# Kernel tuning notes

Measured on AMD Instinct MI355X. Metric: run time of the kernel, lower is better.

The kernel has to match this reference:

```python
import jax, jax.numpy as jnp
import numpy as np

N = 500_000      # nodes
E = 4_000_000    # edges (avg degree 8)
F_IN = 24        # n_input (includeHeading=False, coords=False)
H = 64           # n_hidden
K = 6            # K_block Chebyshev order
OUT = 6          # n_output
EPS = 1e-5       # BatchNorm eps


def setup_inputs() -> dict:
    key = jax.random.key(0)
    ks = jax.random.split(key, 8)
    x = jax.random.normal(ks[0], (N, F_IN), dtype=jnp.float32)
    edge_index = jax.random.randint(ks[1], (2, E), 0, N, dtype=jnp.int32)
    # ChebConv(24 -> 64, K=6): stacked per-order weights [K, F_IN, H] + bias
    W1 = jax.random.normal(ks[2], (K, F_IN, H), dtype=jnp.float32) * (1.0 / np.sqrt(F_IN))
    b1 = jnp.zeros((H,), dtype=jnp.float32)
    # BatchNorm1d(64) affine params
    gamma = jnp.ones((H,), dtype=jnp.float32)
    beta = jnp.zeros((H,), dtype=jnp.float32)
    # conv_mix ChebConv(64 -> 6, K=1)
    Wmix = jax.random.normal(ks[3], (1, H, OUT), dtype=jnp.float32) * (1.0 / np.sqrt(H))
    bmix = jnp.zeros((OUT,), dtype=jnp.float32)
    return {"x": x, "edge_index": edge_index, "W1": W1, "b1": b1,
            "gamma": gamma, "beta": beta, "Wmix": Wmix, "bmix": bmix}


def cheb_conv(x, edge_index, W, b):
    """PyG ChebConv with normalization='sym', lambda_max=2.
    L_hat = L - I = -D^{-1/2} A D^{-1/2} (zero diagonal).
    """
    Kk = W.shape[0]
    row, col = edge_index[0], edge_index[1]  # messages flow row -> col
    deg = jax.ops.segment_sum(jnp.ones((E,), x.dtype), col, num_segments=N)
    dis = jnp.where(deg > 0, jax.lax.rsqrt(jnp.maximum(deg, 1.0)), 0.0)
    norm = -(dis[row] * dis[col])  # [E]

    def prop(h):  # h: [N, F] -> L_hat @ h via gather-scale-scatter
        return jax.ops.segment_sum(norm[:, None] * h[row], col, num_segments=N)

    Tx0 = x
    out = Tx0 @ W[0]
    if Kk > 1:
        Tx1 = prop(Tx0)
        out = out + Tx1 @ W[1]
        for k in range(2, Kk):
            Tx2 = 2.0 * prop(Tx1) - Tx0
            out = out + Tx2 @ W[k]
            Tx0, Tx1 = Tx1, Tx2
    return out + b


def reference(x, edge_index, W1, b1, gamma, beta, Wmix, bmix):
    # Kipfblock: ChebConv -> BatchNorm1d (batch stats) -> ReLU
    h = cheb_conv(x, edge_index, W1, b1)            # [N, H]
    mean = jnp.mean(h, axis=0)
    var = jnp.mean(jnp.square(h - mean), axis=0)    # biased var, as torch BN training
    h = (h - mean) * jax.lax.rsqrt(var + EPS) * gamma + beta
    h = jax.nn.relu(h)
    # conv_mix: ChebConv K=1 reduces to a dense linear (T_0 = x only)
    y = h @ Wmix[0] + bmix                          # [N, OUT]
    # F.dropout is identity in eval mode
    return y
```

## Files before the change

kernel.cpp:

```cpp
#include <hip/hip_runtime.h>
#include <hip/hip_fp16.h>

#define NN 500000
#define NE 4000000
#define FI 24
#define FH 64
#define KC 6
#define FO 6
#define BN_EPS 1e-5f

#define SLOTS 32
#define RH 32
#define NMT (NN / 16)
#define PASS_GRID 1024

#define EPT 8
#define CHUNK (256 * EPT)
#define NCHUNK ((NE + CHUNK - 1) / CHUNK)

#define BUCKETS 512
#define BW 977
#define BCAP 15500

#define RMASK 0x7FFFFu

typedef _Float16 half8 __attribute__((ext_vector_type(8)));
typedef float f32x4 __attribute__((ext_vector_type(4)));
typedef int int4v __attribute__((ext_vector_type(4)));
union U4H8 { uint4 u; half8 h; };


__device__ __forceinline__ void acc8(float* a, float d, uint4 u) {
    const __half2* h2 = (const __half2*)&u;
    #pragma unroll
    for (int j = 0; j < 4; ++j) {
        float2 f = __half22float2(h2[j]);
        a[2 * j]     += d * f.x;
        a[2 * j + 1] += d * f.y;
    }
}

__device__ __forceinline__ uint4 pack8(const float* a) {
    uint4 u;
    __half2* h2 = (__half2*)&u;
    #pragma unroll
    for (int j = 0; j < 4; ++j) h2[j] = __floats2half2_rn(a[2 * j], a[2 * j + 1]);
    return u;
}


__global__ __launch_bounds__(256) void k_scatter(
    const int* __restrict__ row, const int* __restrict__ col,
    unsigned int* __restrict__ ebuf, int* __restrict__ cur) {
    __shared__ unsigned int val[CHUNK];
    __shared__ unsigned short bk[CHUNK];
    __shared__ int hist[BUCKETS], base[BUCKETS], rk[BUCKETS];
    for (int t = threadIdx.x; t < BUCKETS; t += 256) { hist[t] = 0; rk[t] = 0; }
    __syncthreads();
    const int b0 = blockIdx.x * CHUNK;
    #pragma unroll
    for (int i = 0; i < EPT / 4; ++i) {
        int li4 = (i * 256 + threadIdx.x) * 4;
        int e0 = b0 + li4;
        if (e0 + 4 <= NE) {
            int4v c4 = *(const int4v*)(col + e0);
            int4v r4 = *(const int4v*)(row + e0);
            #pragma unroll
            for (int j = 0; j < 4; ++j) {
                int c = c4[j], r = r4[j];
                int b = c / BW, cl = c - b * BW;
                val[li4 + j] = (unsigned int)r | ((unsigned int)cl << 19);
                bk[li4 + j] = (unsigned short)b;
                atomicAdd(&hist[b], 1);
            }
        } else {
            for (int j = 0; j < 4; ++j) {
                int e = e0 + j, li = li4 + j;
                if (e < NE) {
                    int c = col[e], r = row[e];
                    int b = c / BW, cl = c - b * BW;
                    val[li] = (unsigned int)r | ((unsigned int)cl << 19);
                    bk[li] = (unsigned short)b;
                    atomicAdd(&hist[b], 1);
                } else {
                    bk[li] = 0xFFFF;
                }
            }
        }
    }
    __syncthreads();
    for (int t = threadIdx.x; t < BUCKETS; t += 256) {
        int n = hist[t];
        base[t] = n ? atomicAdd(&cur[t], n) : 0;
    }
    __syncthreads();
    #pragma unroll
    for (int i = 0; i < EPT / 4; ++i) {
        int li4 = (i * 256 + threadIdx.x) * 4;
        #pragma unroll
        for (int j = 0; j < 4; ++j) {
            int li = li4 + j;
            int b = bk[li];
            if (b != 0xFFFF) {
                int rkk = atomicAdd(&rk[b], 1);
                int pos = base[b] + rkk;
                if (pos < BCAP) ebuf[(size_t)b * BCAP + pos] = val[li];
            }
        }
    }
}


__global__ __launch_bounds__(256) void k_build(
    const unsigned int* __restrict__ ebuf, const int* __restrict__ cur,
    int* __restrict__ cnt, int* __restrict__ csrcT) {
    __shared__ int cl_cnt[BW];
    const int b = blockIdx.x;
    const int nbase = b * BW;
    const int width = (NN - nbase < BW) ? (NN - nbase) : BW;
    for (int i = threadIdx.x; i < BW; i += 256) cl_cnt[i] = 0;
    __syncthreads();
    int nb = cur[b];
    if (nb > BCAP) nb = BCAP;
    for (int i = threadIdx.x; i < nb; i += 256) {
        unsigned int v = ebuf[(size_t)b * BCAP + i];
        int cl = v >> 19;
        int r = v & RMASK;
        int pos = atomicAdd(&cl_cnt[cl], 1);
        if (pos < SLOTS) csrcT[(size_t)pos * NN + nbase + cl] = r;
    }
    __syncthreads();
    for (int i = threadIdx.x; i < width; i += 256) cnt[nbase + i] = cl_cnt[i];
}

__global__ void k_dis(const int* __restrict__ cnt, float* __restrict__ dis) {
    int n = blockIdx.x * blockDim.x + threadIdx.x;
    if (n < NN) {
        int d = cnt[n];
        dis[n] = d > 0 ? rsqrtf((float)d) : 0.0f;
    }
}


__global__ __launch_bounds__(256) void k_pack(
    const int* __restrict__ cnt, unsigned int* __restrict__ csrcT) {
    int n = blockIdx.x * 256 + threadIdx.x;
    if (n >= NN) return;
    int deg = cnt[n];
    if (deg > SLOTS) deg = SLOTS;
    for (int s = 0; s < deg; ++s) {
        size_t idx = (size_t)s * NN + n;
        unsigned int r = csrcT[idx] & RMASK;
        int dg = cnt[r];
        if (dg > 8191) dg = 8191;
        csrcT[idx] = r | ((unsigned int)dg << 19);
    }
}


__global__ void k_xhalf(const float* __restrict__ x, __half* __restrict__ Th0) {
    int n = blockIdx.x * blockDim.x + threadIdx.x;
    if (n >= NN) return;
    const float* r = x + (size_t)n * FI;
    float v[24];
    #pragma unroll
    for (int i = 0; i < 6; ++i) {
        float4 f = ((const float4*)r)[i];
        v[4 * i] = f.x; v[4 * i + 1] = f.y; v[4 * i + 2] = f.z; v[4 * i + 3] = f.w;
    }
    uint4* o = (uint4*)(Th0 + (size_t)n * RH);
    o[0] = pack8(v); o[1] = pack8(v + 8); o[2] = pack8(v + 16);
    o[3] = make_uint4(0, 0, 0, 0);
}


template<bool FIRST>
__global__ __launch_bounds__(256) void k_prop(
    const int* __restrict__ cnt, const unsigned int* __restrict__ csrcT,
    const float* __restrict__ dis,
    const __half* __restrict__ Tin, const __half* __restrict__ Tpp,
    __half* __restrict__ Tout) {
    int n = blockIdx.x * 256 + threadIdx.x;
    if (n >= NN) return;
    int deg = cnt[n];
    if (deg > SLOTS) deg = SLOTS;
    float a[24];
    #pragma unroll
    for (int j = 0; j < 24; ++j) a[j] = 0.0f;
    int s = 0;
    for (; s + 2 <= deg; s += 2) {
        unsigned int e0 = csrcT[(size_t)s * NN + n];
        unsigned int e1 = csrcT[(size_t)(s + 1) * NN + n];
        unsigned int r0 = e0 & RMASK, r1 = e1 & RMASK;
        unsigned int g0 = e0 >> 19,  g1 = e1 >> 19;
        float d0 = g0 ? rsqrtf((float)g0) : 0.0f;
        float d1 = g1 ? rsqrtf((float)g1) : 0.0f;
        const uint4* p0 = (const uint4*)(Tin + (size_t)r0 * RH);
        const uint4* p1 = (const uint4*)(Tin + (size_t)r1 * RH);
        uint4 u00 = p0[0], u01 = p0[1], u02 = p0[2];
        uint4 u10 = p1[0], u11 = p1[1], u12 = p1[2];
        acc8(a, d0, u00); acc8(a + 8, d0, u01); acc8(a + 16, d0, u02);
        acc8(a, d1, u10); acc8(a + 8, d1, u11); acc8(a + 16, d1, u12);
    }
    if (s < deg) {
        unsigned int e0 = csrcT[(size_t)s * NN + n];
        unsigned int r0 = e0 & RMASK;
        unsigned int g0 = e0 >> 19;
        float d0 = g0 ? rsqrtf((float)g0) : 0.0f;
        const uint4* p0 = (const uint4*)(Tin + (size_t)r0 * RH);
        acc8(a, d0, p0[0]); acc8(a + 8, d0, p0[1]); acc8(a + 16, d0, p0[2]);
    }
    float m = FIRST ? -dis[n] : -2.0f * dis[n];
    if (FIRST) {
        #pragma unroll
        for (int j = 0; j < 24; ++j) a[j] *= m;
    } else {
        const uint4* pr = (const uint4*)(Tpp + (size_t)n * RH);
        uint4 p0 = pr[0], p1 = pr[1], p2 = pr[2];
        float pv[24];
        {
            const __half2* h2 = (const __half2*)&p0;
            #pragma unroll
            for (int j = 0; j < 4; ++j) { float2 f = __half22float2(h2[j]); pv[2*j] = f.x; pv[2*j+1] = f.y; }
        }
        {
            const __half2* h2 = (const __half2*)&p1;
            #pragma unroll
            for (int j = 0; j < 4; ++j) { float2 f = __half22float2(h2[j]); pv[8+2*j] = f.x; pv[8+2*j+1] = f.y; }
        }
        {
            const __half2* h2 = (const __half2*)&p2;
            #pragma unroll
            for (int j = 0; j < 4; ++j) { float2 f = __half22float2(h2[j]); pv[16+2*j] = f.x; pv[16+2*j+1] = f.y; }
        }
        #pragma unroll
        for (int j = 0; j < 24; ++j) a[j] = m * a[j] - pv[j];
    }
    uint4* o = (uint4*)(Tout + (size_t)n * RH);
    o[0] = pack8(a); o[1] = pack8(a + 8); o[2] = pack8(a + 16);
    o[3] = make_uint4(0, 0, 0, 0);
}


__device__ __forceinline__ void build_bfrags(const float* __restrict__ W1, uint4* Bf) {
    for (int s = threadIdx.x; s < KC * 4 * 64; s += 256) {
        int lane = s & 63, blk = s >> 6;
        int seg = blk >> 2, nb = blk & 3;
        int q = lane >> 4, n = lane & 15;
        float v[8];
        #pragma unroll
        for (int j = 0; j < 8; ++j) {
            int k = q * 8 + j;
            v[j] = (k < FI) ? W1[(seg * FI + k) * FH + nb * 16 + n] : 0.0f;
        }
        U4H8 u;
        __half2* h2 = (__half2*)&u;
        #pragma unroll
        for (int j = 0; j < 4; ++j) h2[j] = __floats2half2_rn(v[2 * j], v[2 * j + 1]);
        Bf[s] = u.u;
    }
}

__global__ __launch_bounds__(256) void k_pass1(
    const __half* __restrict__ Th, const float* __restrict__ W1,
    const float* __restrict__ b1, float* __restrict__ stats,
    __half* __restrict__ h) {
    __shared__ uint4 Bf[KC * 4 * 64];
    __shared__ float st[2 * FH];
    build_bfrags(W1, Bf);
    if (threadIdx.x < 2 * FH) st[threadIdx.x] = 0.0f;
    __syncthreads();
    const int lane = threadIdx.x & 63;
    const int q = lane >> 4, ln = lane & 15;
    const int wid = blockIdx.x * 4 + (threadIdx.x >> 6);
    const int nw = gridDim.x * 4;
    float bias[4];
    #pragma unroll
    for (int nb = 0; nb < 4; ++nb) bias[nb] = b1[nb * 16 + ln];
    float ssum[4] = {0, 0, 0, 0}, sqsum[4] = {0, 0, 0, 0};
    for (int t = wid; t < NMT; t += nw) {
        const int n0 = t * 16;
        f32x4 acc[4];
        #pragma unroll
        for (int nb = 0; nb < 4; ++nb)
            acc[nb] = (f32x4){bias[nb], bias[nb], bias[nb], bias[nb]};
        #pragma unroll
        for (int seg = 0; seg < KC; ++seg) {
            U4H8 a;
            a.u = *(const uint4*)(Th + (size_t)seg * ((size_t)NN * RH)
                                  + (size_t)(n0 + ln) * RH + q * 8);
            #pragma unroll
            for (int nb = 0; nb < 4; ++nb) {
                U4H8 b; b.u = Bf[(seg * 4 + nb) * 64 + lane];
                acc[nb] = __builtin_amdgcn_mfma_f32_16x16x32_f16(a.h, b.h, acc[nb], 0, 0, 0);
            }
        }
        #pragma unroll
        for (int nb = 0; nb < 4; ++nb) {
            #pragma unroll
            for (int r = 0; r < 4; ++r) {
                float v = acc[nb][r];
                ssum[nb] += v;
                sqsum[nb] += v * v;
                h[(size_t)(n0 + q * 4 + r) * FH + nb * 16 + ln] = __float2half(v);
            }
        }
    }
    #pragma unroll
    for (int nb = 0; nb < 4; ++nb) {
        ssum[nb]  += __shfl_xor(ssum[nb], 16);  ssum[nb]  += __shfl_xor(ssum[nb], 32);
        sqsum[nb] += __shfl_xor(sqsum[nb], 16); sqsum[nb] += __shfl_xor(sqsum[nb], 32);
    }
    if (lane < 16) {
        #pragma unroll
        for (int nb = 0; nb < 4; ++nb) {
            atomicAdd(&st[nb * 16 + ln], ssum[nb]);
            atomicAdd(&st[FH + nb * 16 + ln], sqsum[nb]);
        }
    }
    __syncthreads();
    if (threadIdx.x < 2 * FH) atomicAdd(&stats[threadIdx.x], st[threadIdx.x]);
}

__global__ void k_finalize(const float* __restrict__ stats, const float* __restrict__ gamma,
                           const float* __restrict__ beta, float* __restrict__ ss) {
    int f = threadIdx.x;
    if (f < FH) {
        float mean = stats[f] * (1.0f / NN);
        float var  = stats[f + FH] * (1.0f / NN) - mean * mean;
        float rstd = rsqrtf(var + BN_EPS);
        float sc = gamma[f] * rstd;
        ss[f] = sc;
        ss[f + FH] = beta[f] - mean * sc;
    }
}


__global__ __launch_bounds__(256) void k_pass2(
    const __half* __restrict__ h, const float* __restrict__ ss,
    const float* __restrict__ Wmix, const float* __restrict__ bmix,
    float* __restrict__ y) {
    __shared__ float tab[FH * 8];
    for (int f = threadIdx.x; f < FH; f += 256) {
        tab[f * 8 + 0] = ss[f];
        tab[f * 8 + 1] = ss[FH + f];
        #pragma unroll
        for (int o = 0; o < FO; ++o) tab[f * 8 + 2 + o] = Wmix[f * FO + o];
    }
    __syncthreads();
    int n = blockIdx.x * 256 + threadIdx.x;
    if (n >= NN) return;
    const uint4* hr = (const uint4*)(h + (size_t)n * FH);
    float p[FO];
    #pragma unroll
    for (int o = 0; o < FO; ++o) p[o] = bmix[o];
    #pragma unroll
    for (int blk = 0; blk < 8; ++blk) {
        U4H8 u; u.u = hr[blk];
        const __half2* h2 = (const __half2*)&u;
        #pragma unroll
        for (int j = 0; j < 4; ++j) {
            float2 f2 = __half22float2(h2[j]);
            int f = blk * 8 + j * 2;
            {
                float4 t0 = *(const float4*)&tab[f * 8];
                float4 t1 = *(const float4*)&tab[f * 8 + 4];
                float hv = fmaxf(f2.x * t0.x + t0.y, 0.0f);
                p[0] += hv * t0.z; p[1] += hv * t0.w;
                p[2] += hv * t1.x; p[3] += hv * t1.y;
                p[4] += hv * t1.z; p[5] += hv * t1.w;
            }
            {
                float4 t0 = *(const float4*)&tab[(f + 1) * 8];
                float4 t1 = *(const float4*)&tab[(f + 1) * 8 + 4];
                float hv = fmaxf(f2.y * t0.x + t0.y, 0.0f);
                p[0] += hv * t0.z; p[1] += hv * t0.w;
                p[2] += hv * t1.x; p[3] += hv * t1.y;
                p[4] += hv * t1.z; p[5] += hv * t1.w;
            }
        }
    }
    float* yo = y + (size_t)n * FO;
    #pragma unroll
    for (int o = 0; o < FO; ++o) yo[o] = p[o];
}


extern "C" void kernel_launch(void* const* d_in, const int* in_sizes, int n_in,
                              void* d_out, int out_size, void* d_ws, size_t ws_size,
                              hipStream_t stream) {
    const float* x     = (const float*)d_in[0];
    const int*   edge  = (const int*)d_in[1];
    const float* W1    = (const float*)d_in[2];
    const float* b1    = (const float*)d_in[3];
    const float* gamma = (const float*)d_in[4];
    const float* beta  = (const float*)d_in[5];
    const float* Wmix  = (const float*)d_in[6];
    const float* bmix  = (const float*)d_in[7];
    float* y = (float*)d_out;

    const int* row = edge;
    const int* col = edge + NE;

    const size_t O_CNT   = 0;
    const size_t O_DIS   = 500000;
    const size_t O_STATS = 1000000;
    const size_t O_SS    = 1000128;
    const size_t O_CSRC  = 1000256;
    const size_t O_TH    = 17000256;
    const size_t TOTAL_ELEMS = O_TH + 6ull * NN * RH / 2;
    if (ws_size < TOTAL_ELEMS * 4ull) return;

    float* wf = (float*)d_ws;
    int*   wi = (int*)d_ws;
    int*   cnt   = wi + O_CNT;
    float* dis   = wf + O_DIS;
    float* stats = wf + O_STATS;
    float* ss    = wf + O_SS;
    int*   csrcT = wi + O_CSRC;
    __half* hbuf = (__half*)(wi + O_CSRC);
    __half* Th   = (__half*)(wf + O_TH);
    __half* Th0  = Th;
    __half* Th1  = Th + 1ull * NN * RH;
    __half* Th2  = Th + 2ull * NN * RH;
    __half* Th3  = Th + 3ull * NN * RH;
    __half* Th4  = Th + 4ull * NN * RH;
    __half* Th5  = Th + 5ull * NN * RH;

    unsigned int* ebuf = (unsigned int*)Th5;
    int* cur = (int*)(ebuf + (size_t)BUCKETS * BCAP);

    (void)hipMemsetAsync(cur,   0, BUCKETS * sizeof(int), stream);
    (void)hipMemsetAsync(stats, 0, 128 * sizeof(float), stream);

    const int BS = 256;
    const int GN = (NN + BS - 1) / BS;

    k_scatter<<<NCHUNK, BS, 0, stream>>>(row, col, ebuf, cur);
    k_build<<<BUCKETS, BS, 0, stream>>>(ebuf, cur, cnt, csrcT);
    k_dis<<<GN, BS, 0, stream>>>(cnt, dis);
    k_pack<<<GN, BS, 0, stream>>>(cnt, (unsigned int*)csrcT);
    k_xhalf<<<GN, BS, 0, stream>>>(x, Th0);

    k_prop<true ><<<GN, BS, 0, stream>>>(cnt, (const unsigned int*)csrcT, dis, Th0, nullptr, Th1);
    k_prop<false><<<GN, BS, 0, stream>>>(cnt, (const unsigned int*)csrcT, dis, Th1, Th0, Th2);
    k_prop<false><<<GN, BS, 0, stream>>>(cnt, (const unsigned int*)csrcT, dis, Th2, Th1, Th3);
    k_prop<false><<<GN, BS, 0, stream>>>(cnt, (const unsigned int*)csrcT, dis, Th3, Th2, Th4);
    k_prop<false><<<GN, BS, 0, stream>>>(cnt, (const unsigned int*)csrcT, dis, Th4, Th3, Th5);

    k_pass1<<<PASS_GRID, 256, 0, stream>>>(Th, W1, b1, stats, hbuf);
    k_finalize<<<1, 64, 0, stream>>>(stats, gamma, beta, ss);
    k_pass2<<<GN, 256, 0, stream>>>(hbuf, ss, Wmix, bmix, y);
}
```

Baseline: 765.5 us.

## Renumber nodes by in-degree so prop threads in a wave share loop length

Result: slower. 1.407 ms (+83.9%).

```diff
diff --git a/kernel.cpp b/kernel.cpp
--- a/kernel.cpp
+++ b/kernel.cpp
@@ -12,7 +12,7 @@
 #define SLOTS 32
 #define RH 32
 #define NMT (NN / 16)
-#define PASS_GRID 1024
+#define PASS_GRID 2048
 
 #define EPT 8
 #define CHUNK (256 * EPT)
@@ -20,7 +20,7 @@
 
 #define BUCKETS 512
 #define BW 977
-#define BCAP 15500
+#define NBIN 33
 
 #define RMASK 0x7FFFFu
 
@@ -49,8 +49,90 @@
 }
 
 
+__global__ __launch_bounds__(256) void k_deg(
+    const int* __restrict__ col, int* __restrict__ cnt_raw) {
+    int e0 = (blockIdx.x * 256 + threadIdx.x) * 4;
+    if (e0 + 4 <= NE) {
+        int4v c4 = *(const int4v*)(col + e0);
+        #pragma unroll
+        for (int j = 0; j < 4; ++j) atomicAdd(&cnt_raw[c4[j]], 1);
+    } else {
+        for (int j = 0; j < 4; ++j)
+            if (e0 + j < NE) atomicAdd(&cnt_raw[col[e0 + j]], 1);
+    }
+}
+
+__global__ __launch_bounds__(256) void k_hist(
+    const int* __restrict__ cnt_raw, int* __restrict__ bins) {
+    __shared__ int lb[NBIN];
+    if (threadIdx.x < NBIN) lb[threadIdx.x] = 0;
+    __syncthreads();
+    int n = blockIdx.x * 256 + threadIdx.x;
+    if (n < NN) {
+        int d = cnt_raw[n];
+        if (d > 32) d = 32;
+        atomicAdd(&lb[d], 1);
+    }
+    __syncthreads();
+    if (threadIdx.x < NBIN && lb[threadIdx.x])
+        atomicAdd(&bins[threadIdx.x], lb[threadIdx.x]);
+}
+
+__global__ void k_scan(const int* __restrict__ bins, int* __restrict__ binbase) {
+    if (threadIdx.x == 0) {
+        int acc = 0;
+        for (int i = 0; i < NBIN; ++i) { binbase[i] = acc; acc += bins[i]; }
+    }
+}
+
+__global__ __launch_bounds__(256) void k_rank(
+    const int* __restrict__ cnt_raw, const int* __restrict__ binbase,
+    int* __restrict__ binoff, int* __restrict__ rank, int* __restrict__ bedges) {
+    __shared__ int lc[NBIN], lbase[NBIN];
+    if (threadIdx.x < NBIN) { lc[threadIdx.x] = 0; lbase[threadIdx.x] = 0; }
+    __syncthreads();
+    int n = blockIdx.x * 256 + threadIdx.x;
+    int d = 0, de = 0, lpos = 0;
+    bool valid = (n < NN);
+    if (valid) {
+        de = cnt_raw[n];
+        d = de > 32 ? 32 : de;
+        lpos = atomicAdd(&lc[d], 1);
+    }
+    __syncthreads();
+    if (threadIdx.x < NBIN && lc[threadIdx.x])
+        lbase[threadIdx.x] = atomicAdd(&binoff[threadIdx.x], lc[threadIdx.x]);
+    __syncthreads();
+    if (valid) {
+        int rid = binbase[d] + lbase[d] + lpos;
+        rank[n] = rid;
+        atomicAdd(&bedges[rid / BW], de);
+    }
+}
+
+__global__ __launch_bounds__(512) void k_scan2(
+    const int* __restrict__ bedges, int* __restrict__ bbase, int* __restrict__ cur) {
+    __shared__ int s[BUCKETS];
+    int t = threadIdx.x;
+    int own = bedges[t];
+    s[t] = own;
+    __syncthreads();
+    for (int off = 1; off < BUCKETS; off <<= 1) {
+        int v = (t >= off) ? s[t - off] : 0;
+        __syncthreads();
+        s[t] += v;
+        __syncthreads();
+    }
+    int excl = s[t] - own;
+    bbase[t] = excl;
+    cur[t] = excl;
+    if (t == BUCKETS - 1) bbase[BUCKETS] = s[t];
+}
+
+
 __global__ __launch_bounds__(256) void k_scatter(
     const int* __restrict__ row, const int* __restrict__ col,
+    const int* __restrict__ rank,
     unsigned int* __restrict__ ebuf, int* __restrict__ cur) {
     __shared__ unsigned int val[CHUNK];
     __shared__ unsigned short bk[CHUNK];
@@ -67,9 +149,10 @@
             int4v r4 = *(const int4v*)(row + e0);
             #pragma unroll
             for (int j = 0; j < 4; ++j) {
-                int c = c4[j], r = r4[j];
-                int b = c / BW, cl = c - b * BW;
-                val[li4 + j] = (unsigned int)r | ((unsigned int)cl << 19);
+                int rc = rank[c4[j]];
+                int rr = rank[r4[j]];
+                int b = rc / BW, cl = rc - b * BW;
+                val[li4 + j] = (unsigned int)rr | ((unsigned int)cl << 19);
                 bk[li4 + j] = (unsigned short)b;
                 atomicAdd(&hist[b], 1);
             }
@@ -77,9 +160,10 @@
             for (int j = 0; j < 4; ++j) {
                 int e = e0 + j, li = li4 + j;
                 if (e < NE) {
-                    int c = col[e], r = row[e];
-                    int b = c / BW, cl = c - b * BW;
-                    val[li] = (unsigned int)r | ((unsigned int)cl << 19);
+                    int rc = rank[col[e]];
+                    int rr = rank[row[e]];
+                    int b = rc / BW, cl = rc - b * BW;
+                    val[li] = (unsigned int)rr | ((unsigned int)cl << 19);
                     bk[li] = (unsigned short)b;
                     atomicAdd(&hist[b], 1);
                 } else {
@@ -102,9 +186,8 @@
             int li = li4 + j;
             int b = bk[li];
             if (b != 0xFFFF) {
-                int rkk = atomicAdd(&rk[b], 1);
-                int pos = base[b] + rkk;
-                if (pos < BCAP) ebuf[(size_t)b * BCAP + pos] = val[li];
+                int pos = base[b] + atomicAdd(&rk[b], 1);
+                if (pos < NE) ebuf[pos] = val[li];
             }
         }
     }
@@ -112,22 +195,21 @@
 
 
 __global__ __launch_bounds__(256) void k_build(
-    const unsigned int* __restrict__ ebuf, const int* __restrict__ cur,
+    const unsigned int* __restrict__ ebuf, const int* __restrict__ bbase,
     int* __restrict__ cnt, int* __restrict__ csrcT) {
     __shared__ int cl_cnt[BW];
-    const int b = blockIdx.x;
+    const int b = (BUCKETS - 1) - (int)blockIdx.x;
     const int nbase = b * BW;
     const int width = (NN - nbase < BW) ? (NN - nbase) : BW;
     for (int i = threadIdx.x; i < BW; i += 256) cl_cnt[i] = 0;
     __syncthreads();
-    int nb = cur[b];
-    if (nb > BCAP) nb = BCAP;
-    for (int i = threadIdx.x; i < nb; i += 256) {
-        unsigned int v = ebuf[(size_t)b * BCAP + i];
+    const int beg = bbase[b], end = bbase[b + 1];
+    for (int i = beg + threadIdx.x; i < end; i += 256) {
+        unsigned int v = ebuf[i];
         int cl = v >> 19;
-        int r = v & RMASK;
+        int rr = v & RMASK;
         int pos = atomicAdd(&cl_cnt[cl], 1);
-        if (pos < SLOTS) csrcT[(size_t)pos * NN + nbase + cl] = r;
+        if (pos < SLOTS) csrcT[(size_t)pos * NN + nbase + cl] = rr;
     }
     __syncthreads();
     for (int i = threadIdx.x; i < width; i += 256) cnt[nbase + i] = cl_cnt[i];
@@ -140,7 +222,6 @@
         dis[n] = d > 0 ? rsqrtf((float)d) : 0.0f;
     }
 }
-
 
 __global__ __launch_bounds__(256) void k_pack(
     const int* __restrict__ cnt, unsigned int* __restrict__ csrcT) {
@@ -157,8 +238,8 @@
     }
 }
 
-
-__global__ void k_xhalf(const float* __restrict__ x, __half* __restrict__ Th0) {
+__global__ void k_xhalf(const float* __restrict__ x, const int* __restrict__ rank,
+                        __half* __restrict__ Th0) {
     int n = blockIdx.x * blockDim.x + threadIdx.x;
     if (n >= NN) return;
     const float* r = x + (size_t)n * FI;
@@ -168,11 +249,11 @@
         float4 f = ((const float4*)r)[i];
         v[4 * i] = f.x; v[4 * i + 1] = f.y; v[4 * i + 2] = f.z; v[4 * i + 3] = f.w;
     }
-    uint4* o = (uint4*)(Th0 + (size_t)n * RH);
+    int rid = rank[n];
+    uint4* o = (uint4*)(Th0 + (size_t)rid * RH);
     o[0] = pack8(v); o[1] = pack8(v + 8); o[2] = pack8(v + 16);
     o[3] = make_uint4(0, 0, 0, 0);
 }
-
 
 template<bool FIRST>
 __global__ __launch_bounds__(256) void k_prop(
@@ -241,7 +322,6 @@
     o[3] = make_uint4(0, 0, 0, 0);
 }
 
-
 __device__ __forceinline__ void build_bfrags(const float* __restrict__ W1, uint4* Bf) {
     for (int s = threadIdx.x; s < KC * 4 * 64; s += 256) {
         int lane = s & 63, blk = s >> 6;
@@ -335,9 +415,9 @@
     }
 }
 
-
 __global__ __launch_bounds__(256) void k_pass2(
-    const __half* __restrict__ h, const float* __restrict__ ss,
+    const __half* __restrict__ h, const int* __restrict__ rank,
+    const float* __restrict__ ss,
     const float* __restrict__ Wmix, const float* __restrict__ bmix,
     float* __restrict__ y) {
     __shared__ float tab[FH * 8];
@@ -350,7 +430,8 @@
     __syncthreads();
     int n = blockIdx.x * 256 + threadIdx.x;
     if (n >= NN) return;
-    const uint4* hr = (const uint4*)(h + (size_t)n * FH);
+    int rid = rank[n];
+    const uint4* hr = (const uint4*)(h + (size_t)rid * FH);
     float p[FO];
     #pragma unroll
     for (int o = 0; o < FO; ++o) p[o] = bmix[o];
@@ -406,18 +487,35 @@
     const size_t O_DIS   = 500000;
     const size_t O_STATS = 1000000;
     const size_t O_SS    = 1000128;
-    const size_t O_CSRC  = 1000256;
-    const size_t O_TH    = 17000256;
-    const size_t TOTAL_ELEMS = O_TH + 6ull * NN * RH / 2;
+    const size_t O_AUX   = 1000256;
+    const size_t A_CNTRAW  = O_AUX;
+    const size_t A_RANK    = O_AUX + 500000;
+    const size_t A_BINS    = O_AUX + 1000000;
+    const size_t A_BINBASE = O_AUX + 1000064;
+    const size_t A_BINOFF  = O_AUX + 1000128;
+    const size_t A_BEDGES  = O_AUX + 1000192;
+    const size_t A_BBASE   = O_AUX + 1000704;
+    const size_t A_CUR     = O_AUX + 1001232;
+    const size_t O_CSRC  = O_AUX + 1001760;
+    const size_t O_TH    = O_CSRC + 16000000;
+    const size_t TOTAL_ELEMS = O_TH + 24000000;
     if (ws_size < TOTAL_ELEMS * 4ull) return;
 
     float* wf = (float*)d_ws;
     int*   wi = (int*)d_ws;
-    int*   cnt   = wi + O_CNT;
-    float* dis   = wf + O_DIS;
-    float* stats = wf + O_STATS;
-    float* ss    = wf + O_SS;
-    int*   csrcT = wi + O_CSRC;
+    int*   cnt     = wi + O_CNT;
+    float* dis     = wf + O_DIS;
+    float* stats   = wf + O_STATS;
+    float* ss      = wf + O_SS;
+    int*   cnt_raw = wi + A_CNTRAW;
+    int*   rank    = wi + A_RANK;
+    int*   bins    = wi + A_BINS;
+    int*   binbase = wi + A_BINBASE;
+    int*   binoff  = wi + A_BINOFF;
+    int*   bedges  = wi + A_BEDGES;
+    int*   bbase   = wi + A_BBASE;
+    int*   cur     = wi + A_CUR;
+    int*   csrcT   = wi + O_CSRC;
     __half* hbuf = (__half*)(wi + O_CSRC);
     __half* Th   = (__half*)(wf + O_TH);
     __half* Th0  = Th;
@@ -428,19 +526,27 @@
     __half* Th5  = Th + 5ull * NN * RH;
 
     unsigned int* ebuf = (unsigned int*)Th5;
-    int* cur = (int*)(ebuf + (size_t)BUCKETS * BCAP);
-
-    (void)hipMemsetAsync(cur,   0, BUCKETS * sizeof(int), stream);
-    (void)hipMemsetAsync(stats, 0, 128 * sizeof(float), stream);
+
+    (void)hipMemsetAsync(cnt_raw, 0, NN * sizeof(int), stream);
+    (void)hipMemsetAsync(bins,    0, 64 * sizeof(int), stream);
+    (void)hipMemsetAsync(binoff,  0, 64 * sizeof(int), stream);
+    (void)hipMemsetAsync(bedges,  0, 512 * sizeof(int), stream);
+    (void)hipMemsetAsync(stats,   0, 128 * sizeof(float), stream);
 
     const int BS = 256;
     const int GN = (NN + BS - 1) / BS;
-
-    k_scatter<<<NCHUNK, BS, 0, stream>>>(row, col, ebuf, cur);
-    k_build<<<BUCKETS, BS, 0, stream>>>(ebuf, cur, cnt, csrcT);
+    const int GD = (NE / 4 + BS - 1) / BS;
+
+    k_deg<<<GD, BS, 0, stream>>>(col, cnt_raw);
+    k_hist<<<GN, BS, 0, stream>>>(cnt_raw, bins);
+    k_scan<<<1, 64, 0, stream>>>(bins, binbase);
+    k_rank<<<GN, BS, 0, stream>>>(cnt_raw, binbase, binoff, rank, bedges);
+    k_scan2<<<1, 512, 0, stream>>>(bedges, bbase, cur);
+    k_scatter<<<NCHUNK, BS, 0, stream>>>(row, col, rank, ebuf, cur);
+    k_build<<<BUCKETS, BS, 0, stream>>>(ebuf, bbase, cnt, csrcT);
     k_dis<<<GN, BS, 0, stream>>>(cnt, dis);
     k_pack<<<GN, BS, 0, stream>>>(cnt, (unsigned int*)csrcT);
-    k_xhalf<<<GN, BS, 0, stream>>>(x, Th0);
+    k_xhalf<<<GN, BS, 0, stream>>>(x, rank, Th0);
 
     k_prop<true ><<<GN, BS, 0, stream>>>(cnt, (const unsigned int*)csrcT, dis, Th0, nullptr, Th1);
     k_prop<false><<<GN, BS, 0, stream>>>(cnt, (const unsigned int*)csrcT, dis, Th1, Th0, Th2);
@@ -450,5 +556,5 @@
 
     k_pass1<<<PASS_GRID, 256, 0, stream>>>(Th, W1, b1, stats, hbuf);
     k_finalize<<<1, 64, 0, stream>>>(stats, gamma, beta, ss);
-    k_pass2<<<GN, 256, 0, stream>>>(hbuf, ss, Wmix, bmix, y);
-}
+    k_pass2<<<GN, 256, 0, stream>>>(hbuf, rank, ss, Wmix, bmix, y);
+}
```

## Sort neighbor lists and sweep source-index ranges in lockstep for gather locality

Applied to the files above, without the earlier changes.

After: 816.4 us. +6.7%, slower.

```diff
diff --git a/kernel.cpp b/kernel.cpp
--- a/kernel.cpp
+++ b/kernel.cpp
@@ -23,6 +23,7 @@
 #define BCAP 15500
 
 #define RMASK 0x7FFFFu
+#define NRANGE 16
 
 typedef _Float16 half8 __attribute__((ext_vector_type(8)));
 typedef float f32x4 __attribute__((ext_vector_type(4)));
@@ -142,18 +143,26 @@
 }
 
 
-__global__ __launch_bounds__(256) void k_pack(
+__global__ __launch_bounds__(256) void k_packsort(
     const int* __restrict__ cnt, unsigned int* __restrict__ csrcT) {
+    __shared__ unsigned int buf[256 * 33];
     int n = blockIdx.x * 256 + threadIdx.x;
     if (n >= NN) return;
+    unsigned int* b = &buf[threadIdx.x * 33];
     int deg = cnt[n];
     if (deg > SLOTS) deg = SLOTS;
+    for (int s = 0; s < deg; ++s) b[s] = csrcT[(size_t)s * NN + n];
+    for (int i = 1; i < deg; ++i) {
+        unsigned int v = b[i];
+        int j = i - 1;
+        while (j >= 0 && b[j] > v) { b[j + 1] = b[j]; --j; }
+        b[j + 1] = v;
+    }
     for (int s = 0; s < deg; ++s) {
-        size_t idx = (size_t)s * NN + n;
-        unsigned int r = csrcT[idx] & RMASK;
+        unsigned int r = b[s];
         int dg = cnt[r];
         if (dg > 8191) dg = 8191;
-        csrcT[idx] = r | ((unsigned int)dg << 19);
+        csrcT[(size_t)s * NN + n] = r | ((unsigned int)dg << 19);
     }
 }
 
@@ -188,27 +197,18 @@
     #pragma unroll
     for (int j = 0; j < 24; ++j) a[j] = 0.0f;
     int s = 0;
-    for (; s + 2 <= deg; s += 2) {
-        unsigned int e0 = csrcT[(size_t)s * NN + n];
-        unsigned int e1 = csrcT[(size_t)(s + 1) * NN + n];
-        unsigned int r0 = e0 & RMASK, r1 = e1 & RMASK;
-        unsigned int g0 = e0 >> 19,  g1 = e1 >> 19;
-        float d0 = g0 ? rsqrtf((float)g0) : 0.0f;
-        float d1 = g1 ? rsqrtf((float)g1) : 0.0f;
-        const uint4* p0 = (const uint4*)(Tin + (size_t)r0 * RH);
-        const uint4* p1 = (const uint4*)(Tin + (size_t)r1 * RH);
-        uint4 u00 = p0[0], u01 = p0[1], u02 = p0[2];
-        uint4 u10 = p1[0], u11 = p1[1], u12 = p1[2];
-        acc8(a, d0, u00); acc8(a + 8, d0, u01); acc8(a + 16, d0, u02);
-        acc8(a, d1, u10); acc8(a + 8, d1, u11); acc8(a + 16, d1, u12);
-    }
-    if (s < deg) {
-        unsigned int e0 = csrcT[(size_t)s * NN + n];
-        unsigned int r0 = e0 & RMASK;
-        unsigned int g0 = e0 >> 19;
-        float d0 = g0 ? rsqrtf((float)g0) : 0.0f;
-        const uint4* p0 = (const uint4*)(Tin + (size_t)r0 * RH);
-        acc8(a, d0, p0[0]); acc8(a + 8, d0, p0[1]); acc8(a + 16, d0, p0[2]);
+    unsigned int e = deg ? csrcT[n] : 0;
+    #pragma unroll 1
+    for (int p = 0; p < NRANGE; ++p) {
+        while (s < deg && (int)((e & RMASK) >> 15) == p) {
+            unsigned int g = e >> 19;
+            float d = g ? rsqrtf((float)g) : 0.0f;
+            const uint4* pr = (const uint4*)(Tin + (size_t)(e & RMASK) * RH);
+            uint4 u0 = pr[0], u1 = pr[1], u2 = pr[2];
+            ++s;
+            e = (s < deg) ? csrcT[(size_t)s * NN + n] : 0;
+            acc8(a, d, u0); acc8(a + 8, d, u1); acc8(a + 16, d, u2);
+        }
     }
     float m = FIRST ? -dis[n] : -2.0f * dis[n];
     if (FIRST) {
@@ -439,7 +439,7 @@
     k_scatter<<<NCHUNK, BS, 0, stream>>>(row, col, ebuf, cur);
     k_build<<<BUCKETS, BS, 0, stream>>>(ebuf, cur, cnt, csrcT);
     k_dis<<<GN, BS, 0, stream>>>(cnt, dis);
-    k_pack<<<GN, BS, 0, stream>>>(cnt, (unsigned int*)csrcT);
+    k_packsort<<<GN, BS, 0, stream>>>(cnt, (unsigned int*)csrcT);
     k_xhalf<<<GN, BS, 0, stream>>>(x, Th0);
 
     k_prop<true ><<<GN, BS, 0, stream>>>(cnt, (const unsigned int*)csrcT, dis, Th0, nullptr, Th1);
```
